# Performance work log

Measured on AMD Instinct MI355X. Metric: run time of the kernel, lower is better.

The kernel has to match this reference:

```python
import jax, jax.numpy as jnp
import numpy as np

D = 1024
H = 16
DH = D // H  # 64
FF_H = 4096
EPS = 1e-5


def layernorm(x, gamma, beta):
    mu = jnp.mean(x, axis=-1, keepdims=True)
    var = jnp.var(x, axis=-1, keepdims=True)
    return (x - mu) * jax.lax.rsqrt(var + EPS) * gamma + beta


def setup_inputs() -> dict:
    key = jax.random.key(0)
    ks = jax.random.split(key, 12)
    B, S = 2, 2048
    q = jax.random.normal(ks[0], (B, S, D), dtype=jnp.float32)
    k = jax.random.normal(ks[1], (B, S, D), dtype=jnp.float32)
    v = jax.random.normal(ks[2], (B, S, D), dtype=jnp.float32)
    time_lengths = jax.random.randint(ks[3], (B,), 0, S)
    mask = jnp.zeros((1, 1, S, S), dtype=jnp.float32)
    sc = 0.02
    Wq = jax.random.normal(ks[4], (D, D), dtype=jnp.float32) * sc
    Wk = jax.random.normal(ks[5], (D, D), dtype=jnp.float32) * sc
    Wv = jax.random.normal(ks[6], (D, D), dtype=jnp.float32) * sc
    Wd = jax.random.normal(ks[7], (D, D), dtype=jnp.float32) * sc
    W1 = jax.random.normal(ks[8], (D, FF_H), dtype=jnp.float32) * sc
    b1 = jnp.zeros((FF_H,), dtype=jnp.float32)
    W2 = jax.random.normal(ks[9], (FF_H, D), dtype=jnp.float32) * sc
    b2 = jnp.zeros((D,), dtype=jnp.float32)
    g1 = jnp.ones((D,), dtype=jnp.float32)
    be1 = jnp.zeros((D,), dtype=jnp.float32)
    g2 = jnp.ones((D,), dtype=jnp.float32)
    be2 = jnp.zeros((D,), dtype=jnp.float32)
    return {"q": q, "k": k, "v": v, "time_lengths": time_lengths, "mask": mask,
            "Wq": Wq, "Wk": Wk, "Wv": Wv, "Wd": Wd,
            "W1": W1, "b1": b1, "W2": W2, "b2": b2,
            "g1": g1, "be1": be1, "g2": g2, "be2": be2}


def reference(q, k, v, time_lengths, mask, Wq, Wk, Wv, Wd, W1, b1, W2, b2, g1, be1, g2, be2):
    B, S, _ = q.shape
    scale = jnp.sqrt(jnp.float32(DH))
    # project and split heads: [B,H,S,DH]
    qh = (q @ Wq).reshape(B, S, H, DH).transpose(0, 2, 1, 3)
    kh = (k @ Wk).reshape(B, S, H, DH).transpose(0, 2, 1, 3)
    vh = (v @ Wv).reshape(B, S, H, DH).transpose(0, 2, 1, 3)
    score = jnp.einsum('bhqd,bhkd->bhqk', qh, kh) / scale + mask
    attn = jax.nn.softmax(score, axis=-1)
    z = jnp.einsum('bhqk,bhkd->bhqd', attn, vh)
    z = z.transpose(0, 2, 1, 3).reshape(B, S, D)
    z = z @ Wd
    # Add & LayerNorm 1 (note: original applies LN to attn out, then adds q)
    x = layernorm(z, g1, be1) + q
    # FF (dropout is identity in eval)
    ff = jax.nn.relu(x @ W1 + b1) @ W2 + b2
    return layernorm(ff + x, g2, be2)
```

## Files before the change

kernel.cpp:

```cpp
#include <hip/hip_runtime.h>
#include <hip/hip_bf16.h>


#define SEQ 2048
#define DM  1024
#define LNEPS 1e-5f

typedef __attribute__((ext_vector_type(8))) short bf16x8;
typedef __attribute__((ext_vector_type(4))) float f32x4;

#define GAS __attribute__((address_space(1)))
#define LAS __attribute__((address_space(3)))

static __device__ __forceinline__ void gl_lds16(const unsigned short* g, unsigned short* l) {
    __builtin_amdgcn_global_load_lds((const GAS void*)g, (LAS void*)l, 16, 0, 0);
}

static __device__ __forceinline__ unsigned short f2bf(float f) {
    unsigned u = __builtin_bit_cast(unsigned, f);
    u += 0x7fffu + ((u >> 16) & 1u);
    return (unsigned short)(u >> 16);
}

static __device__ __forceinline__ unsigned cvt_pk_bf16(float lo, float hi) {
    unsigned r;
    asm("v_cvt_pk_bf16_f32 %0, %1, %2" : "=v"(r) : "v"(lo), "v"(hi));
    return r;
}

__global__ __launch_bounds__(512) void gemm256(
    const unsigned short* __restrict__ A, const unsigned short* __restrict__ Bt,
    unsigned short* __restrict__ Cb,
    int N, int Klen, int lda, int ldb,
    const float* __restrict__ bias, int ep, int lgn)
{
    __shared__ unsigned short Asl[2][2][128 * 64];
    __shared__ unsigned short Bsl[2][2][128 * 64];

    const int t = threadIdx.x, lane = t & 63, w = t >> 6;
    const int wm = w >> 2, wn = w & 3;
    const int l15 = lane & 15, l16 = lane >> 4;

    const int nwg = gridDim.x;
    const int sw = (blockIdx.x & 7) * (nwg >> 3) + (blockIdx.x >> 3);
    const int n0 = (sw & ((1 << lgn) - 1)) * 256;
    const int m0 = (sw >> lgn) * 256;

    const int sr = t >> 3, sc = t & 7;
    const int gcs = (sc ^ (sr & 7)) * 8;

    f32x4 acc[8][4];
    #pragma unroll
    for (int i = 0; i < 8; i++)
        #pragma unroll
        for (int j = 0; j < 4; j++)
            acc[i][j] = (f32x4){0.f, 0.f, 0.f, 0.f};

    auto STAGEPAIR = [&](int kt, int ph) {
        const int slot = kt & 1;
        if (ph < 2) {
            #pragma unroll
            for (int p = 0; p < 2; p++)
                gl_lds16(&A[(size_t)(m0 + ph * 128 + p * 64 + sr) * lda + kt * 64 + gcs],
                         &Asl[slot][ph][p * 4096 + w * 512]);
        } else {
            const int h = ph - 2;
            #pragma unroll
            for (int p = 0; p < 2; p++)
                gl_lds16(&Bt[(size_t)(n0 + h * 128 + p * 64 + sr) * ldb + kt * 64 + gcs],
                         &Bsl[slot][h][p * 4096 + w * 512]);
        }
    };

    #pragma unroll
    for (int ph = 0; ph < 4; ph++) STAGEPAIR(0, ph);

    const int NT = Klen >> 6;
    for (int T = 0; T < NT; T++) {
        const int slot = T & 1;
        const int Tn = (T + 1 < NT) ? T + 1 : 0;

        bf16x8 afr[4][2], bfr[2][2];

        auto LOADA = [&](int MH) {
            #pragma unroll
            for (int mi = 0; mi < 4; mi++)
                #pragma unroll
                for (int kk = 0; kk < 2; kk++) {
                    const int r = MH * 64 + mi * 16 + l15;
                    afr[mi][kk] = *(const bf16x8*)
                        &Asl[slot][wm][r * 64 + (((kk * 4 + l16) ^ (r & 7)) * 8)];
                }
        };
        auto LOADB = [&](int NH) {
            #pragma unroll
            for (int ni = 0; ni < 2; ni++)
                #pragma unroll
                for (int kk = 0; kk < 2; kk++) {
                    const int r = (wn & 1) * 64 + NH * 32 + ni * 16 + l15;
                    bfr[ni][kk] = *(const bf16x8*)
                        &Bsl[slot][wn >> 1][r * 64 + (((kk * 4 + l16) ^ (r & 7)) * 8)];
                }
        };
        auto MFMA16 = [&](int MH, int NH) {
            __builtin_amdgcn_s_setprio(1);
            #pragma unroll
            for (int mi = 0; mi < 4; mi++)
                #pragma unroll
                for (int ni = 0; ni < 2; ni++) {
                    acc[MH * 4 + mi][NH * 2 + ni] = __builtin_amdgcn_mfma_f32_16x16x32_bf16(
                        afr[mi][0], bfr[ni][0], acc[MH * 4 + mi][NH * 2 + ni], 0, 0, 0);
                    acc[MH * 4 + mi][NH * 2 + ni] = __builtin_amdgcn_mfma_f32_16x16x32_bf16(
                        afr[mi][1], bfr[ni][1], acc[MH * 4 + mi][NH * 2 + ni], 0, 0, 0);
                }
            __builtin_amdgcn_s_setprio(0);
        };

        STAGEPAIR(Tn, 0);
        asm volatile("s_waitcnt vmcnt(2)" ::: "memory");
        __builtin_amdgcn_s_barrier();
        __builtin_amdgcn_sched_barrier(0);
        LOADA(0); LOADB(0);
        asm volatile("s_waitcnt lgkmcnt(0)" ::: "memory");
        __builtin_amdgcn_sched_barrier(0);
        MFMA16(0, 0);
        __builtin_amdgcn_s_barrier();

        STAGEPAIR(Tn, 1);
        __builtin_amdgcn_s_barrier();
        __builtin_amdgcn_sched_barrier(0);
        LOADB(1);
        asm volatile("s_waitcnt lgkmcnt(0)" ::: "memory");
        __builtin_amdgcn_sched_barrier(0);
        MFMA16(0, 1);
        __builtin_amdgcn_s_barrier();

        STAGEPAIR(Tn, 2);
        __builtin_amdgcn_s_barrier();
        __builtin_amdgcn_sched_barrier(0);
        LOADA(1);
        asm volatile("s_waitcnt lgkmcnt(0)" ::: "memory");
        __builtin_amdgcn_sched_barrier(0);
        MFMA16(1, 1);
        __builtin_amdgcn_s_barrier();

        STAGEPAIR(Tn, 3);
        __builtin_amdgcn_s_barrier();
        __builtin_amdgcn_sched_barrier(0);
        LOADB(0);
        asm volatile("s_waitcnt lgkmcnt(0)" ::: "memory");
        __builtin_amdgcn_sched_barrier(0);
        MFMA16(1, 0);
        __builtin_amdgcn_s_barrier();
    }

    asm volatile("s_waitcnt vmcnt(0)" ::: "memory");

    #pragma unroll
    for (int f = 0; f < 8; f++) {
        const int row0 = m0 + wm * 128 + (f >> 2) * 64 + (f & 3) * 16 + l16 * 4;
        #pragma unroll
        for (int g = 0; g < 4; g++) {
            const int col = n0 + wn * 64 + (g >> 1) * 32 + (g & 1) * 16 + l15;
            const float bv = ep ? bias[col] : 0.f;
            #pragma unroll
            for (int r = 0; r < 4; r++) {
                float vv = acc[f][g][r] + bv;
                if (ep == 2) vv = fmaxf(vv, 0.f);
                Cb[(size_t)(row0 + r) * N + col] = f2bf(vv);
            }
        }
    }
}

__global__ __launch_bounds__(256) void gemm_bf16(
    const unsigned short* __restrict__ A, const unsigned short* __restrict__ Bt,
    float* __restrict__ Cf, unsigned short* __restrict__ Cb,
    unsigned short* __restrict__ CbT,
    int M, int N, int Klen, int lda, int ldb,
    size_t sA, size_t sB, size_t sC,
    const float* __restrict__ bias, int ep, int lgn)
{
    __shared__ unsigned short As[2][128 * 32];
    __shared__ unsigned short Bs[2][128 * 32];

    const int t = threadIdx.x, lane = t & 63, w = t >> 6;
    const int wm = w >> 1, wn = w & 1;

    const int nwg = gridDim.x;
    const int sw = (blockIdx.x & 7) * (nwg >> 3) + (blockIdx.x >> 3);
    const int n0 = (sw & ((1 << lgn) - 1)) * 128;
    const int m0 = (sw >> lgn) * 128;

    A  += (size_t)blockIdx.z * sA;
    Bt += (size_t)blockIdx.z * sB;
    const size_t cbase = (size_t)blockIdx.z * sC;
    const int l15 = lane & 15, l16 = lane >> 4;
    const int ar = lane >> 2, ac = (lane & 3) * 8;

    f32x4 acc[4][4];
    #pragma unroll
    for (int i = 0; i < 4; i++)
        #pragma unroll
        for (int j = 0; j < 4; j++)
            acc[i][j] = (f32x4){0.f, 0.f, 0.f, 0.f};

    auto stage = [&](int buf, int k0) {
        #pragma unroll
        for (int i = 0; i < 2; i++) {
            const int rg = w * 2 + i;
            gl_lds16(&A [(size_t)(m0 + rg * 16 + ar) * lda + k0 + ac], &As[buf][rg * 512]);
            gl_lds16(&Bt[(size_t)(n0 + rg * 16 + ar) * ldb + k0 + ac], &Bs[buf][rg * 512]);
        }
    };
    auto compute = [&](int buf) {
        bf16x8 af[4], bfr[4];
        #pragma unroll
        for (int i = 0; i < 4; i++) {
            af[i]  = *(const bf16x8*)&As[buf][(wm * 64 + i * 16 + l15) * 32 + l16 * 8];
            bfr[i] = *(const bf16x8*)&Bs[buf][(wn * 64 + i * 16 + l15) * 32 + l16 * 8];
        }
        #pragma unroll
        for (int mi = 0; mi < 4; mi++)
            #pragma unroll
            for (int ni = 0; ni < 4; ni++)
                acc[mi][ni] = __builtin_amdgcn_mfma_f32_16x16x32_bf16(
                    af[mi], bfr[ni], acc[mi][ni], 0, 0, 0);
    };

    stage(0, 0);
    __syncthreads();
    int k0 = 0;
    for (; k0 + 32 < Klen; k0 += 32) {
        const int cur = (k0 >> 5) & 1;
        stage(cur ^ 1, k0 + 32);
        compute(cur);
        __syncthreads();
    }
    compute((k0 >> 5) & 1);

    if (CbT && blockIdx.z == 2) {
        #pragma unroll
        for (int ni = 0; ni < 4; ni++) {
            const int col = n0 + wn * 64 + ni * 16 + l15;
            const int hh = col >> 6, d = col & 63;
            #pragma unroll
            for (int mi = 0; mi < 4; mi++) {
                const int row = m0 + wm * 64 + mi * 16 + l16 * 4;
                const int bb = row >> 11, s = row & 2047;
                ushort4 o;
                o.x = f2bf(acc[mi][ni][0]); o.y = f2bf(acc[mi][ni][1]);
                o.z = f2bf(acc[mi][ni][2]); o.w = f2bf(acc[mi][ni][3]);
                *(ushort4*)&CbT[((size_t)((bb * 16 + hh) * 64 + d)) * SEQ + s] = o;
            }
        }
        return;
    }

    #pragma unroll
    for (int ni = 0; ni < 4; ni++) {
        const int col = n0 + wn * 64 + ni * 16 + l15;
        const float bv = (ep && blockIdx.z == 0) ? bias[col] : 0.f;
        #pragma unroll
        for (int mi = 0; mi < 4; mi++) {
            #pragma unroll
            for (int r = 0; r < 4; r++) {
                const int row = m0 + wm * 64 + mi * 16 + l16 * 4 + r;
                float vv = acc[mi][ni][r] + bv;
                if (ep == 2) vv = fmaxf(vv, 0.f);
                if (Cf) Cf[cbase + (size_t)row * N + col] = vv;
                else    Cb[cbase + (size_t)row * N + col] = f2bf(vv);
            }
        }
    }
}

__global__ __launch_bounds__(512) void attn_mfma(
    const unsigned short* __restrict__ qh, const unsigned short* __restrict__ kh,
    const unsigned short* __restrict__ vhT, const float* __restrict__ mask,
    unsigned short* __restrict__ z)
{
    __shared__ unsigned short Ks0[64 * 64];
    __shared__ unsigned short Ks1[64 * 64];
    __shared__ unsigned short Vst[64 * 64];
    __shared__ unsigned short Ps[128 * 72];

    const int t = threadIdx.x, lane = t & 63, w = t >> 6;
    const int bid = blockIdx.x;
    const int qt = bid >> 5, h = bid & 15, b = (bid >> 4) & 1;
    const int q0 = qt * 128, qr = w * 16;
    const int l15 = lane & 15, l16 = lane >> 4;

    const int lr = lane >> 3;
    const int gc = ((lane & 7) ^ lr) * 8;

    const size_t qbase = (size_t)(b * SEQ + q0) * DM + h * 64;
    const size_t kbase = (size_t)(b * SEQ) * DM + h * 64;
    const size_t vbase = (size_t)((b * 16 + h) * 64) * SEQ;

    #pragma unroll
    for (int i = 0; i < 2; i++) {
        const int rg = w * 2 + i;
        gl_lds16(&qh[qbase + (size_t)(rg * 8 + lr) * DM + gc], &Ps[rg * 512]);
    }
    gl_lds16(&kh[kbase + (size_t)(w * 8 + lr) * DM + gc], &Ks0[w * 512]);
    __syncthreads();

    const int sw0 = ((l16    ) ^ (l15 & 7)) * 8;
    const int sw1 = ((l16 + 4) ^ (l15 & 7)) * 8;
    const bf16x8 bQ0 = *(const bf16x8*)&Ps[(qr + l15) * 64 + sw0];
    const bf16x8 bQ1 = *(const bf16x8*)&Ps[(qr + l15) * 64 + sw1];
    __syncthreads();

    const float* mrow = mask + (size_t)(q0 + qr + l15) * SEQ;

    float m_i = -1e30f, l_i = 0.f;
    f32x4 o4[4];
    #pragma unroll
    for (int mi = 0; mi < 4; mi++) o4[mi] = (f32x4){0.f, 0.f, 0.f, 0.f};

    for (int kt = 0; kt < SEQ / 64; kt++) {
        const int k0 = kt * 64;
        const int kn = ((kt + 1) & (SEQ / 64 - 1)) * 64;
        unsigned short* Kcur = (kt & 1) ? Ks1 : Ks0;
        unsigned short* Knxt = (kt & 1) ? Ks0 : Ks1;

        __builtin_amdgcn_s_barrier();

        float4 mv[4];
        #pragma unroll
        for (int ki = 0; ki < 4; ki++)
            mv[ki] = *(const float4*)&mrow[k0 + ki * 16 + l16 * 4];

        gl_lds16(&vhT[vbase + (size_t)(w * 8 + lr) * SEQ + k0 + gc], &Vst[w * 512]);
        __builtin_amdgcn_sched_barrier(0);
        gl_lds16(&kh[kbase + (size_t)(kn + w * 8 + lr) * DM + gc], &Knxt[w * 512]);

        asm volatile("s_waitcnt vmcnt(6)" ::: "memory");
        __builtin_amdgcn_s_barrier();
        __builtin_amdgcn_sched_barrier(0);

        f32x4 s4[4];
        __builtin_amdgcn_s_setprio(1);
        #pragma unroll
        for (int ki = 0; ki < 4; ki++) {
            const int r = ki * 16 + l15;
            const bf16x8 aK0 = *(const bf16x8*)&Kcur[r * 64 + sw0];
            const bf16x8 aK1 = *(const bf16x8*)&Kcur[r * 64 + sw1];
            f32x4 a0 = (f32x4){0.f, 0.f, 0.f, 0.f};
            a0 = __builtin_amdgcn_mfma_f32_16x16x32_bf16(aK0, bQ0, a0, 0, 0, 0);
            s4[ki] = __builtin_amdgcn_mfma_f32_16x16x32_bf16(aK1, bQ1, a0, 0, 0, 0);
        }
        __builtin_amdgcn_s_setprio(0);

        float sv[16];
        #pragma unroll
        for (int ki = 0; ki < 4; ki++) {
            sv[ki * 4 + 0] = s4[ki][0] * 0.125f + mv[ki].x;
            sv[ki * 4 + 1] = s4[ki][1] * 0.125f + mv[ki].y;
            sv[ki * 4 + 2] = s4[ki][2] * 0.125f + mv[ki].z;
            sv[ki * 4 + 3] = s4[ki][3] * 0.125f + mv[ki].w;
        }

        float rm = fmaxf(sv[0], sv[1]);
        #pragma unroll
        for (int i = 2; i < 16; i += 2) rm = fmaxf(fmaxf(rm, sv[i]), sv[i + 1]);
        rm = fmaxf(rm, __shfl_xor(rm, 16));
        rm = fmaxf(rm, __shfl_xor(rm, 32));

        const bool skip = __all(rm <= m_i + 8.f);
        float mnew = m_i, alpha = 1.f;
        if (!skip) { mnew = fmaxf(m_i, rm); alpha = __expf(m_i - mnew); }

        float ps = 0.f;
        #pragma unroll
        for (int ki = 0; ki < 4; ki++) {
            const float p0 = __expf(sv[ki * 4 + 0] - mnew);
            const float p1 = __expf(sv[ki * 4 + 1] - mnew);
            const float p2 = __expf(sv[ki * 4 + 2] - mnew);
            const float p3 = __expf(sv[ki * 4 + 3] - mnew);
            ps += (p0 + p1) + (p2 + p3);
            uint2 pk;
            pk.x = cvt_pk_bf16(p0, p1);
            pk.y = cvt_pk_bf16(p2, p3);
            *(uint2*)&Ps[(qr + l15) * 72 + ki * 16 + l16 * 4] = pk;
        }
        ps += __shfl_xor(ps, 16);
        ps += __shfl_xor(ps, 32);
        if (!skip) {
            m_i = mnew;
            l_i = l_i * alpha + ps;
            #pragma unroll
            for (int mi = 0; mi < 4; mi++)
                #pragma unroll
                for (int r = 0; r < 4; r++) o4[mi][r] *= alpha;
        } else {
            l_i += ps;
        }

        asm volatile("s_waitcnt vmcnt(1)" ::: "memory");
        __builtin_amdgcn_s_barrier();
        __builtin_amdgcn_sched_barrier(0);

        const bf16x8 bP0 = *(const bf16x8*)&Ps[(qr + l15) * 72 + l16 * 8];
        const bf16x8 bP1 = *(const bf16x8*)&Ps[(qr + l15) * 72 + 32 + l16 * 8];
        __builtin_amdgcn_s_setprio(1);
        #pragma unroll
        for (int mi = 0; mi < 4; mi++) {
            const int r = mi * 16 + l15;
            const bf16x8 aV0 = *(const bf16x8*)&Vst[r * 64 + sw0];
            const bf16x8 aV1 = *(const bf16x8*)&Vst[r * 64 + sw1];
            o4[mi] = __builtin_amdgcn_mfma_f32_16x16x32_bf16(aV0, bP0, o4[mi], 0, 0, 0);
            o4[mi] = __builtin_amdgcn_mfma_f32_16x16x32_bf16(aV1, bP1, o4[mi], 0, 0, 0);
        }
        __builtin_amdgcn_s_setprio(0);
    }

    asm volatile("s_waitcnt vmcnt(0)" ::: "memory");

    const float inv = 1.f / l_i;
    #pragma unroll
    for (int mi = 0; mi < 4; mi++) {
        const float a0 = o4[mi][0] * inv, a1 = o4[mi][1] * inv;
        const float a2 = o4[mi][2] * inv, a3 = o4[mi][3] * inv;
        uint2 ov;
        ov.x = cvt_pk_bf16(a0, a1);
        ov.y = cvt_pk_bf16(a2, a3);
        *(uint2*)&z[(size_t)(b * SEQ + q0 + qr + l15) * DM + h * 64 + mi * 16 + l16 * 4] = ov;
    }
}

__global__ __launch_bounds__(256) void prep(
    const float* __restrict__ q, const float* __restrict__ k, const float* __restrict__ v,
    unsigned short* __restrict__ qb,
    const float* __restrict__ Wq, const float* __restrict__ Wk,
    const float* __restrict__ Wv, const float* __restrict__ Wd,
    const float* __restrict__ W1, const float* __restrict__ W2,
    unsigned short* __restrict__ Wqt, unsigned short* __restrict__ Wdt,
    unsigned short* __restrict__ W1t, unsigned short* __restrict__ W2t)
{
    const int z = blockIdx.z, t = threadIdx.x;
    const int flat = blockIdx.y * 64 + blockIdx.x;

    if (z < 3) {
        const float* src = z == 0 ? q : (z == 1 ? k : v);
        unsigned short* dst = qb + (size_t)z * ((size_t)SEQ * 2 * DM);
        const size_t base = (size_t)flat * 4096 + t * 4;
        #pragma unroll
        for (int i = 0; i < 4; i++) {
            const float4 w4 = *(const float4*)&src[base + i * 1024];
            ushort4 o; o.x = f2bf(w4.x); o.y = f2bf(w4.y); o.z = f2bf(w4.z); o.w = f2bf(w4.w);
            *(ushort4*)&dst[base + i * 1024] = o;
        }
        return;
    }

    __shared__ float ts[64][65];
    const float* W; unsigned short* Wt; int K, N, n0, k0;
    if (z < 7) {
        if (flat >= 256) return;
        W  = z == 3 ? Wq : z == 4 ? Wk : (z == 5 ? Wv : Wd);
        Wt = z == 3 ? Wqt : z == 4 ? Wqt + 1024 * 1024
           : z == 5 ? Wqt + 2 * 1024 * 1024 : Wdt;
        K = 1024; N = 1024;
        n0 = (flat & 15) * 64; k0 = (flat >> 4) * 64;
    } else if (z == 7) {
        W = W1; Wt = W1t; K = 1024; N = 4096;
        n0 = blockIdx.x * 64; k0 = blockIdx.y * 64;
    } else {
        W = W2; Wt = W2t; K = 4096; N = 1024;
        n0 = (flat & 15) * 64; k0 = (flat >> 4) * 64;
    }

    const int r = t >> 4, c4 = (t & 15) * 4;
    #pragma unroll
    for (int i = 0; i < 4; i++) {
        const float4 v4 = *(const float4*)&W[(size_t)(k0 + r + i * 16) * N + n0 + c4];
        ts[r + i * 16][c4 + 0] = v4.x; ts[r + i * 16][c4 + 1] = v4.y;
        ts[r + i * 16][c4 + 2] = v4.z; ts[r + i * 16][c4 + 3] = v4.w;
    }
    __syncthreads();
    #pragma unroll
    for (int i = 0; i < 4; i++) {
        const int n = r + i * 16;
        ushort4 o;
        o.x = f2bf(ts[c4 + 0][n]); o.y = f2bf(ts[c4 + 1][n]);
        o.z = f2bf(ts[c4 + 2][n]); o.w = f2bf(ts[c4 + 3][n]);
        *(ushort4*)&Wt[(size_t)(n0 + n) * K + k0 + c4] = o;
    }
}

__global__ __launch_bounds__(256) void ln_res(
    const float* __restrict__ a, const float* __restrict__ a2,
    const float* __restrict__ a3, const float* __restrict__ a4,
    const float* __restrict__ r,
    const float* __restrict__ g, const float* __restrict__ be,
    float* __restrict__ out, unsigned short* __restrict__ outb, int mode)
{
    __shared__ float redls[8];
    const int row = blockIdx.x, t = threadIdx.x;
    const size_t base = (size_t)row * DM;

    float vals[4], s = 0.f, sq = 0.f;
    #pragma unroll
    for (int i = 0; i < 4; i++) {
        const int c = t + 256 * i;
        float x = a[base + c];
        if (a2) x += a2[base + c];
        if (a3) x += a3[base + c];
        if (a4) x += a4[base + c];
        if (mode == 1) x += r[base + c];
        vals[i] = x; s += x; sq += x * x;
    }
    #pragma unroll
    for (int off = 32; off > 0; off >>= 1) { s += __shfl_down(s, off); sq += __shfl_down(sq, off); }
    if ((t & 63) == 0) { redls[t >> 6] = s; redls[4 + (t >> 6)] = sq; }
    __syncthreads();
    s  = redls[0] + redls[1] + redls[2] + redls[3];
    sq = redls[4] + redls[5] + redls[6] + redls[7];

    const float mu  = s * (1.f / 1024.f);
    const float var = sq * (1.f / 1024.f) - mu * mu;
    const float rs  = rsqrtf(var + LNEPS);
    #pragma unroll
    for (int i = 0; i < 4; i++) {
        const int c = t + 256 * i;
        float y = (vals[i] - mu) * rs * g[c] + be[c];
        if (mode == 0) y += r[base + c];
        out[base + c] = y;
        if (outb) outb[base + c] = f2bf(y);
    }
}

extern "C" void kernel_launch(void* const* d_in, const int* in_sizes, int n_in,
                              void* d_out, int out_size, void* d_ws, size_t ws_size,
                              hipStream_t stream)
{
    const float* q    = (const float*)d_in[0];
    const float* k    = (const float*)d_in[1];
    const float* v    = (const float*)d_in[2];
    const float* mask = (const float*)d_in[4];
    const float* Wq   = (const float*)d_in[5];
    const float* Wk   = (const float*)d_in[6];
    const float* Wv   = (const float*)d_in[7];
    const float* Wd   = (const float*)d_in[8];
    const float* W1   = (const float*)d_in[9];
    const float* b1   = (const float*)d_in[10];
    const float* W2   = (const float*)d_in[11];
    const float* b2   = (const float*)d_in[12];
    const float* g1   = (const float*)d_in[13];
    const float* be1  = (const float*)d_in[14];
    const float* g2   = (const float*)d_in[15];
    const float* be2  = (const float*)d_in[16];
    float* out = (float*)d_out;

    char* WS = (char*)d_ws;
    const size_t MiB = 1u << 20;
    const size_t ND  = (size_t)4096 * 1024;

    unsigned short* qb  = (unsigned short*)(WS + 0);
    unsigned short* zb  = (unsigned short*)(WS + 8 * MiB);
    unsigned short* xb  = (unsigned short*)(WS + 16 * MiB);
    unsigned short* Wqt = (unsigned short*)(WS + 24 * MiB);
    unsigned short* Wdt = (unsigned short*)(WS + 30 * MiB);
    unsigned short* W1t = (unsigned short*)(WS + 32 * MiB);
    unsigned short* W2t = (unsigned short*)(WS + 40 * MiB);
    unsigned short* qh  = (unsigned short*)(WS + 48 * MiB);
    unsigned short* vhT = (unsigned short*)(WS + 64 * MiB);
    float*          zd0 = (float*)(WS + 48 * MiB);
    float*          zd1 = (float*)(WS + 64 * MiB);
    float*          x   = (float*)(WS + 80 * MiB);
    unsigned short* h1  = (unsigned short*)(WS + 96 * MiB);
    float*          y0  = (float*)(WS + 48 * MiB);
    float*          y1  = (float*)(WS + 64 * MiB);

    unsigned short* kh = qh + ND;

    const dim3 blk(256);

    prep<<<dim3(64, 16, 9), blk, 0, stream>>>(q, k, v, qb, Wq, Wk, Wv, Wd, W1, W2,
                                              Wqt, Wdt, W1t, W2t);

    gemm_bf16<<<dim3(256, 1, 3), blk, 0, stream>>>(qb, Wqt, nullptr, qh, vhT,
        4096, 1024, 1024, 1024, 1024, ND, (size_t)1024 * 1024, ND, nullptr, 0, 3);

    attn_mfma<<<dim3(512), dim3(512), 0, stream>>>(qh, kh, vhT, mask, zb);

    gemm_bf16<<<dim3(256, 1, 2), blk, 0, stream>>>(zb, Wdt, zd0, nullptr, nullptr,
        4096, 1024, 512, 1024, 1024, 512, 512, ND, nullptr, 0, 3);

    ln_res<<<dim3(4096), blk, 0, stream>>>(zd0, zd1, nullptr, nullptr, q,
                                           g1, be1, x, xb, 0);

    gemm256<<<dim3(256, 1, 1), dim3(512), 0, stream>>>(xb, W1t, h1,
        4096, 1024, 1024, 1024, b1, 2, 4);

    gemm_bf16<<<dim3(256, 1, 2), blk, 0, stream>>>(h1, W2t, y0, nullptr, nullptr,
        4096, 1024, 2048, 4096, 4096, 2048, 2048, ND, b2, 1, 3);

    ln_res<<<dim3(4096), blk, 0, stream>>>(y0, y1, nullptr, nullptr, x,
                                           g2, be2, out, nullptr, 1);
}
```

Measured before the change: 444.8 us.

## Use 256-tile GEMM with 4-way split-K for FFN down-projection; vectorize LayerNorm

The second FFN GEMM moves from the generic 128-tile kernel with 2-way split-K to the 256x256 gemm256 kernel, extended with a fp32 output path and a batched z dimension so it runs as a 4-way split-K writing four partial buffers. The final LayerNorm sums all four partials plus the residual. The ln_res kernel is also rewritten to use float4 loads and stores instead of strided scalar accesses. The larger tiles aim to raise MFMA efficiency and data reuse, at the cost of more partial-sum traffic and a grid of only 256 blocks.

```diff
diff --git a/kernel.cpp b/kernel.cpp
--- a/kernel.cpp
+++ b/kernel.cpp
@@ -30,8 +30,9 @@
 
 __global__ __launch_bounds__(512) void gemm256(
     const unsigned short* __restrict__ A, const unsigned short* __restrict__ Bt,
-    unsigned short* __restrict__ Cb,
+    unsigned short* __restrict__ Cb, float* __restrict__ Cf,
     int N, int Klen, int lda, int ldb,
+    size_t sA, size_t sB, size_t sC, int zskip,
     const float* __restrict__ bias, int ep, int lgn)
 {
     __shared__ unsigned short Asl[2][2][128 * 64];
@@ -45,6 +46,11 @@
     const int sw = (blockIdx.x & 7) * (nwg >> 3) + (blockIdx.x >> 3);
     const int n0 = (sw & ((1 << lgn) - 1)) * 256;
     const int m0 = (sw >> lgn) * 256;
+
+    A  += (size_t)blockIdx.z * sA;
+    Bt += (size_t)blockIdx.z * sB;
+    int zi = blockIdx.z; if (zskip && zi >= 2) zi++;
+    const size_t cbase = (size_t)zi * sC;
 
     const int sr = t >> 3, sc = t & 7;
     const int gcs = (sc ^ (sr & 7)) * 8;
@@ -155,6 +161,22 @@
     }
 
     asm volatile("s_waitcnt vmcnt(0)" ::: "memory");
+
+    if (Cf) {
+        #pragma unroll
+        for (int f = 0; f < 8; f++) {
+            const int row0 = m0 + wm * 128 + (f >> 2) * 64 + (f & 3) * 16 + l16 * 4;
+            #pragma unroll
+            for (int g = 0; g < 4; g++) {
+                const int col = n0 + wn * 64 + (g >> 1) * 32 + (g & 1) * 16 + l15;
+                const float bv = (ep && blockIdx.z == 0) ? bias[col] : 0.f;
+                #pragma unroll
+                for (int r = 0; r < 4; r++)
+                    Cf[cbase + (size_t)(row0 + r) * N + col] = acc[f][g][r] + bv;
+            }
+        }
+        return;
+    }
 
     #pragma unroll
     for (int f = 0; f < 8; f++) {
@@ -500,18 +522,21 @@
     __shared__ float redls[8];
     const int row = blockIdx.x, t = threadIdx.x;
     const size_t base = (size_t)row * DM;
-
-    float vals[4], s = 0.f, sq = 0.f;
-    #pragma unroll
-    for (int i = 0; i < 4; i++) {
-        const int c = t + 256 * i;
-        float x = a[base + c];
-        if (a2) x += a2[base + c];
-        if (a3) x += a3[base + c];
-        if (a4) x += a4[base + c];
-        if (mode == 1) x += r[base + c];
-        vals[i] = x; s += x; sq += x * x;
-    }
+    const int c = t * 4;
+
+    float4 va = *(const float4*)&a[base + c];
+    if (a2) { const float4 v2 = *(const float4*)&a2[base + c];
+              va.x += v2.x; va.y += v2.y; va.z += v2.z; va.w += v2.w; }
+    if (a3) { const float4 v3 = *(const float4*)&a3[base + c];
+              va.x += v3.x; va.y += v3.y; va.z += v3.z; va.w += v3.w; }
+    if (a4) { const float4 v4 = *(const float4*)&a4[base + c];
+              va.x += v4.x; va.y += v4.y; va.z += v4.z; va.w += v4.w; }
+    float4 vr;
+    if (mode == 1) { vr = *(const float4*)&r[base + c];
+                     va.x += vr.x; va.y += vr.y; va.z += vr.z; va.w += vr.w; }
+
+    float s  = (va.x + va.y) + (va.z + va.w);
+    float sq = (va.x * va.x + va.y * va.y) + (va.z * va.z + va.w * va.w);
     #pragma unroll
     for (int off = 32; off > 0; off >>= 1) { s += __shfl_down(s, off); sq += __shfl_down(sq, off); }
     if ((t & 63) == 0) { redls[t >> 6] = s; redls[4 + (t >> 6)] = sq; }
@@ -522,13 +547,23 @@
     const float mu  = s * (1.f / 1024.f);
     const float var = sq * (1.f / 1024.f) - mu * mu;
     const float rs  = rsqrtf(var + LNEPS);
-    #pragma unroll
-    for (int i = 0; i < 4; i++) {
-        const int c = t + 256 * i;
-        float y = (vals[i] - mu) * rs * g[c] + be[c];
-        if (mode == 0) y += r[base + c];
-        out[base + c] = y;
-        if (outb) outb[base + c] = f2bf(y);
+
+    const float4 vg = *(const float4*)&g[c];
+    const float4 vb = *(const float4*)&be[c];
+    float4 y;
+    y.x = (va.x - mu) * rs * vg.x + vb.x;
+    y.y = (va.y - mu) * rs * vg.y + vb.y;
+    y.z = (va.z - mu) * rs * vg.z + vb.z;
+    y.w = (va.w - mu) * rs * vg.w + vb.w;
+    if (mode == 0) {
+        vr = *(const float4*)&r[base + c];
+        y.x += vr.x; y.y += vr.y; y.z += vr.z; y.w += vr.w;
+    }
+    *(float4*)&out[base + c] = y;
+    if (outb) {
+        ushort4 o;
+        o.x = f2bf(y.x); o.y = f2bf(y.y); o.z = f2bf(y.z); o.w = f2bf(y.w);
+        *(ushort4*)&outb[base + c] = o;
     }
 }
 
@@ -571,8 +606,10 @@
     float*          zd1 = (float*)(WS + 64 * MiB);
     float*          x   = (float*)(WS + 80 * MiB);
     unsigned short* h1  = (unsigned short*)(WS + 96 * MiB);
-    float*          y0  = (float*)(WS + 48 * MiB);
-    float*          y1  = (float*)(WS + 64 * MiB);
+    float*          y0  = (float*)(WS + 0);
+    float*          y1  = (float*)(WS + 16 * MiB);
+    float*          y2  = (float*)(WS + 48 * MiB);
+    float*          y3  = (float*)(WS + 64 * MiB);
 
     unsigned short* kh = qh + ND;
 
@@ -592,12 +629,11 @@
     ln_res<<<dim3(4096), blk, 0, stream>>>(zd0, zd1, nullptr, nullptr, q,
                                            g1, be1, x, xb, 0);
 
-    gemm256<<<dim3(256, 1, 1), dim3(512), 0, stream>>>(xb, W1t, h1,
-        4096, 1024, 1024, 1024, b1, 2, 4);
-
-    gemm_bf16<<<dim3(256, 1, 2), blk, 0, stream>>>(h1, W2t, y0, nullptr, nullptr,
-        4096, 1024, 2048, 4096, 4096, 2048, 2048, ND, b2, 1, 3);
-
-    ln_res<<<dim3(4096), blk, 0, stream>>>(y0, y1, nullptr, nullptr, x,
-                                           g2, be2, out, nullptr, 1);
-}
+    gemm256<<<dim3(256, 1, 1), dim3(512), 0, stream>>>(xb, W1t, h1, nullptr,
+        4096, 1024, 1024, 1024, 0, 0, 0, 0, b1, 2, 4);
+
+    gemm256<<<dim3(64, 1, 4), dim3(512), 0, stream>>>(h1, W2t, nullptr, (float*)WS,
+        1024, 1024, 4096, 4096, 1024, 1024, (size_t)4 * 1024 * 1024, 1, b2, 1, 2);
+
+    ln_res<<<dim3(4096), blk, 0, stream>>>(y0, y1, y2, y3, x, g2, be2, out, nullptr, 1);
+}
```

After: 433.5 us. 1.03x faster.
